# Kernel optimization log

Hardware: AMD Instinct MI355X
Metric: run time of the kernel (lower is better)

The kernel has to match this reference:

```python
import jax, jax.numpy as jnp
import numpy as np

H, DK, OUT = 8, 32, 256
SQRT_DK = float(np.sqrt(DK))


def _proj(feat, W, b):
    # (N, in) -> (N, H, DK)
    return (feat @ W + b).reshape(feat.shape[0], H, DK)


def _rel(k_src, v_src, q_dst, src, dst, att_w, msg_w, pri, n_dst):
    # HGT-style per-relation edge attention + segment softmax + aggregation.
    key = jnp.einsum('ehd,hdk->ehk', k_src[src], att_w)          # (E,H,DK)
    att = (q_dst[dst] * key).sum(-1) * pri / SQRT_DK             # (E,H)
    val = jnp.einsum('ehd,hdk->ehk', v_src[src], msg_w)          # (E,H,DK)
    m = jax.ops.segment_max(att, dst, num_segments=n_dst)
    m = jnp.where(jnp.isfinite(m), m, 0.0)
    e = jnp.exp(att - m[dst])
    s = jax.ops.segment_sum(e, dst, num_segments=n_dst)
    alpha = e / jnp.maximum(s[dst], 1e-9)
    h = jax.ops.segment_sum(alpha[..., None] * val, dst, num_segments=n_dst)
    return jax.nn.relu(h.reshape(n_dst, OUT))                    # relu per etype (reduce_func)


def _ln(x, g, b):
    mu = x.mean(-1, keepdims=True)
    var = ((x - mu) ** 2).mean(-1, keepdims=True)
    return (x - mu) / jnp.sqrt(var + 1e-5) * g + b


def _forward(feat_word, feat_topic, feat_doc, Wk, bk, Wq, bq, Wv, bv, Wa, ba,
             ln_scale, ln_bias, skip, rel_pri, rel_att, rel_msg,
             src_ww, dst_ww, src_wt, dst_wt, src_wd, dst_wd,
             src_tt, dst_tt, src_td, dst_td):
    # ntype order: word=0, topic=1, doc=2; etype order: ww=0, wt=1, wd=2, tt=3, td=4
    Nw, Nt, Nd = feat_word.shape[0], feat_topic.shape[0], feat_doc.shape[0]
    k_w, q_w, v_w = _proj(feat_word, Wk[0], bk[0]), _proj(feat_word, Wq[0], bq[0]), _proj(feat_word, Wv[0], bv[0])
    k_t, q_t, v_t = _proj(feat_topic, Wk[1], bk[1]), _proj(feat_topic, Wq[1], bq[1]), _proj(feat_topic, Wv[1], bv[1])
    q_d = _proj(feat_doc, Wq[2], bq[2])
    t_ww = _rel(k_w, v_w, q_w, src_ww, dst_ww, rel_att[0], rel_msg[0], rel_pri[0], Nw)
    t_wt = _rel(k_w, v_w, q_t, src_wt, dst_wt, rel_att[1], rel_msg[1], rel_pri[1], Nt)
    t_wd = _rel(k_w, v_w, q_d, src_wd, dst_wd, rel_att[2], rel_msg[2], rel_pri[2], Nd)
    t_tt = _rel(k_t, v_t, q_t, src_tt, dst_tt, rel_att[3], rel_msg[3], rel_pri[3], Nt)
    t_td = _rel(k_t, v_t, q_d, src_td, dst_td, rel_att[4], rel_msg[4], rel_pri[4], Nd)
    # cross_reducer='mean' across etypes targeting each ntype
    t_word, t_topic, t_doc = t_ww, (t_wt + t_tt) * 0.5, (t_wd + t_td) * 0.5
    outs = []
    for i, (t, feat) in enumerate([(t_word, feat_word), (t_topic, feat_topic), (t_doc, feat_doc)]):
        a = jax.nn.sigmoid(skip[i])
        trans = (t @ Wa[i] + ba[i]) * a + feat * (1.0 - a)
        outs.append(_ln(trans, ln_scale[i], ln_bias[i]))
    return jnp.concatenate(outs, axis=0)  # (Nw+Nt+Nd, OUT)


def setup_inputs() -> dict:
    key = jax.random.key(0)
    ks = jax.random.split(key, 32)
    Nw, Nt, Nd, D = 20000, 2000, 5000, 256
    E = {'ww': (150000, Nw, Nw), 'wt': (80000, Nw, Nt), 'wd': (80000, Nw, Nd),
         'tt': (20000, Nt, Nt), 'td': (40000, Nt, Nd)}
    inp = {
        'feat_word': jax.random.normal(ks[0], (Nw, D), jnp.float32),
        'feat_topic': jax.random.normal(ks[1], (Nt, D), jnp.float32),
        'feat_doc': jax.random.normal(ks[2], (Nd, D), jnp.float32),
        'Wk': jax.random.normal(ks[3], (3, D, D), jnp.float32) * 0.05,
        'bk': jax.random.normal(ks[4], (3, D), jnp.float32) * 0.02,
        'Wq': jax.random.normal(ks[5], (3, D, D), jnp.float32) * 0.05,
        'bq': jax.random.normal(ks[6], (3, D), jnp.float32) * 0.02,
        'Wv': jax.random.normal(ks[7], (3, D, D), jnp.float32) * 0.05,
        'bv': jax.random.normal(ks[8], (3, D), jnp.float32) * 0.02,
        'Wa': jax.random.normal(ks[9], (3, D, D), jnp.float32) * 0.05,
        'ba': jax.random.normal(ks[10], (3, D), jnp.float32) * 0.02,
        'ln_scale': jnp.ones((3, D), jnp.float32),
        'ln_bias': jnp.zeros((3, D), jnp.float32),
        'skip': jnp.ones((3,), jnp.float32),
        'rel_pri': jnp.ones((5, H), jnp.float32),
        'rel_att': jax.random.normal(ks[11], (5, H, DK, DK), jnp.float32) * 0.1,
        'rel_msg': jax.random.normal(ks[12], (5, H, DK, DK), jnp.float32) * 0.1,
    }
    for i, (et, (ne, ns, nd)) in enumerate(E.items()):
        inp['src_' + et] = jax.random.randint(ks[13 + 2 * i], (ne,), 0, ns, jnp.int32)
        inp['dst_' + et] = jax.random.randint(ks[14 + 2 * i], (ne,), 0, nd, jnp.int32)
    return inp


def reference(feat_word, feat_topic, feat_doc, Wk, bk, Wq, bq, Wv, bv, Wa, ba,
              ln_scale, ln_bias, skip, rel_pri, rel_att, rel_msg,
              src_ww, dst_ww, src_wt, dst_wt, src_wd, dst_wd,
              src_tt, dst_tt, src_td, dst_td):
    return _forward(feat_word, feat_topic, feat_doc, Wk, bk, Wq, bq, Wv, bv, Wa, ba,
                    ln_scale, ln_bias, skip, rel_pri, rel_att, rel_msg,
                    src_ww, dst_ww, src_wt, dst_wt, src_wd, dst_wd,
                    src_tt, dst_tt, src_td, dst_td)
```

## Files before the change

### kernel.cpp

```cpp
#include <hip/hip_runtime.h>

static constexpr int NW = 20000, NT = 2000, ND = 5000;
static constexpr int E_WW = 150000, E_WT = 80000, E_WD = 80000, E_TT = 20000, E_TD = 40000;

typedef short bf16x8 __attribute__((ext_vector_type(8)));
typedef float f32x4 __attribute__((ext_vector_type(4)));

__device__ __forceinline__ unsigned short f2bf(float f) {
  union { float f; unsigned int u; } c; c.f = f;
  unsigned int u = c.u;
  u += 0x7fffu + ((u >> 16) & 1u);
  return (unsigned short)(u >> 16);
}
__device__ __forceinline__ float bf2f(unsigned short h) {
  union { unsigned int u; float f; } c; c.u = ((unsigned int)h) << 16; return c.f;
}
__device__ __forceinline__ bf16x8 pack8(float4 a, float4 b) {
  bf16x8 r;
  r[0] = (short)f2bf(a.x); r[1] = (short)f2bf(a.y); r[2] = (short)f2bf(a.z); r[3] = (short)f2bf(a.w);
  r[4] = (short)f2bf(b.x); r[5] = (short)f2bf(b.y); r[6] = (short)f2bf(b.z); r[7] = (short)f2bf(b.w);
  return r;
}

struct Pack7 { const float* src[7]; unsigned short* dst[7]; };
__global__ __launch_bounds__(256) void pack_wt7(Pack7 p) {
  __shared__ float tile[32][33];
  const float* W = p.src[blockIdx.x];
  unsigned short* WT = p.dst[blockIdx.x];
  int bk = blockIdx.y * 32, bn = blockIdx.z * 32;
  int tx = threadIdx.x & 31, ty = threadIdx.x >> 5;
#pragma unroll
  for (int i = 0; i < 32; i += 8)
    tile[ty + i][tx] = W[(size_t)(bk + ty + i) * 256 + bn + tx];
  __syncthreads();
#pragma unroll
  for (int i = 0; i < 32; i += 8)
    WT[(size_t)(bn + ty + i) * 256 + bk + tx] = f2bf(tile[tx][ty + i]);
}

__global__ void pack_headw(const float* __restrict__ w, unsigned short* __restrict__ out, int nmat) {
  int t = blockIdx.x * blockDim.x + threadIdx.x;
  if (t >= nmat * 8192) return;
  int m = t >> 13, rem = t & 8191;
  int hc = rem >> 9, idx = rem & 511;
  int lane = idx >> 3, j = idx & 7;
  int h = hc >> 1, c = hc & 1;
  int k = (lane >> 4) * 8 + j, n = c * 16 + (lane & 15);
  out[t] = f2bf(w[(size_t)m * 8192 + h * 1024 + k * 32 + n]);
}

struct EffArgs {
  const float* wq[5]; const float* bq[5];
  unsigned short* dst[5];
  float* beff;
  const float* att;
};
__global__ void wq_eff_kernel(EffArgs a) {
  int t = blockIdx.x * blockDim.x + threadIdx.x;
  if (t < 5 * 65536) {
    int r = t >> 16, rem = t & 65535;
    int n = rem >> 8, kk = rem & 255;
    int h = n >> 5, j = n & 31;
    const float* wrow = a.wq[r] + kk * 256 + h * 32;
    const float* arow = a.att + r * 8192 + h * 1024 + j * 32;
    float s = 0.f;
#pragma unroll
    for (int d = 0; d < 32; d += 4) {
      float4 wv = *(const float4*)(wrow + d);
      float4 av = *(const float4*)(arow + d);
      s += wv.x * av.x + wv.y * av.y + wv.z * av.z + wv.w * av.w;
    }
    a.dst[r][n * 256 + kk] = f2bf(s);
  } else {
    int idx = t - 5 * 65536;
    if (idx < 1280) {
      int r = idx >> 8, n = idx & 255;
      int h = n >> 5, j = n & 31;
      const float* brow = a.bq[r] + h * 32;
      const float* arow = a.att + r * 8192 + h * 1024 + j * 32;
      float s = 0.f;
#pragma unroll
      for (int d = 0; d < 32; d += 4) {
        float4 bv = *(const float4*)(brow + d);
        float4 av = *(const float4*)(arow + d);
        s += bv.x * av.x + bv.y * av.y + bv.z * av.z + bv.w * av.w;
      }
      a.beff[r * 256 + n] = s;
    }
  }
}

struct ProjAll {
  const float* A[3];
  const unsigned short* WT[3];
  const float* bias[3][4];
  unsigned short* outp[3][4];
  int ostride[3][4];
  int M[3], ncolb[3], bcum[4];
};
__global__ __launch_bounds__(256) void proj_all(ProjAll pa) {
  __shared__ unsigned short As[64 * 64];
  __shared__ unsigned short Bs[64 * 64];
  int nt = 0;
  while (nt < 2 && (int)blockIdx.x >= pa.bcum[nt + 1]) nt++;
  int local = blockIdx.x - pa.bcum[nt];
  int ncolb = pa.ncolb[nt];
  int bmi = local / ncolb, bnb = local % ncolb;
  const int bm = bmi * 64, bn = bnb * 64;
  const float* A = pa.A[nt];
  const unsigned short* WT = pa.WT[nt];
  const int M = pa.M[nt];
  const int tid = threadIdx.x, wave = tid >> 6, lane = tid & 63;
  f32x4 acc[4] = {};
  const int ar = wave * 16 + (lane & 15);
  const int swz = lane & 7;
  for (int k0 = 0; k0 < 256; k0 += 64) {
#pragma unroll
    for (int i = 0; i < 2; i++) {
      int c = tid + i * 256;
      int row = c >> 3, sl = c & 7;
      int srow = bm + row;
      float4 a0 = make_float4(0.f, 0.f, 0.f, 0.f), a1 = a0;
      if (srow < M) {
        a0 = *(const float4*)(A + (size_t)srow * 256 + k0 + sl * 8);
        a1 = *(const float4*)(A + (size_t)srow * 256 + k0 + sl * 8 + 4);
      }
      *(bf16x8*)&As[row * 64 + (sl ^ (row & 7)) * 8] = pack8(a0, a1);
      bf16x8 bv = *(const bf16x8*)(WT + (size_t)(bn + row) * 256 + k0 + sl * 8);
      *(bf16x8*)&Bs[row * 64 + (sl ^ (row & 7)) * 8] = bv;
    }
    __syncthreads();
#pragma unroll
    for (int kk = 0; kk < 2; kk++) {
      int slot = kk * 4 + (lane >> 4);
      bf16x8 a = *(const bf16x8*)&As[ar * 64 + ((slot ^ swz) * 8)];
#pragma unroll
      for (int nf = 0; nf < 4; nf++) {
        int br = nf * 16 + (lane & 15);
        bf16x8 b = *(const bf16x8*)&Bs[br * 64 + ((slot ^ swz) * 8)];
        acc[nf] = __builtin_amdgcn_mfma_f32_16x16x32_bf16(a, b, acc[nf], 0, 0, 0);
      }
    }
    __syncthreads();
  }
  const int col = lane & 15;
  const int seg = bnb >> 2;
  const float* bias = pa.bias[nt][seg];
  unsigned short* outp = pa.outp[nt][seg];
  const int ostride = pa.ostride[nt][seg];
  const int cbase = (bnb & 3) * 64;
#pragma unroll
  for (int nf = 0; nf < 4; nf++) {
    float bsv = bias[cbase + nf * 16 + col];
#pragma unroll
    for (int rr = 0; rr < 4; rr++) {
      int row = bm + wave * 16 + (lane >> 4) * 4 + rr;
      if (row < M)
        outp[(size_t)row * ostride + cbase + nf * 16 + col] = f2bf(acc[nf][rr] + bsv);
    }
  }
}

struct CsrDesc {
  const int* dst[5];
  const int* src[5];
  int E[5], N[5], cbase[5];
};

__global__ void hist5(CsrDesc d, int* __restrict__ counts) {
  int t = blockIdx.x * blockDim.x + threadIdx.x;
  int r = 0, base = 0;
  while (r < 5 && t >= base + d.E[r]) { base += d.E[r]; r++; }
  if (r >= 5) return;
  int e = t - base;
  atomicAdd(counts + d.cbase[r] + d.dst[r][e], 1);
}

__global__ __launch_bounds__(1024) void scan_all(const int* __restrict__ cnt,
                                                 int* __restrict__ off, int N) {
  __shared__ int wpart[16];
  __shared__ int carry_s;
  int tid = threadIdx.x, lane = tid & 63, w = tid >> 6;
  if (tid == 0) carry_s = 0;
  __syncthreads();
  for (int base = 0; base < N; base += 4096) {
    int idx = base + tid * 4;
    int v0 = 0, v1 = 0, v2 = 0, v3 = 0;
    if (idx + 3 < N) {
      int4 t4 = *(const int4*)(cnt + idx);
      v0 = t4.x; v1 = t4.y; v2 = t4.z; v3 = t4.w;
    } else if (idx < N) {
      v0 = cnt[idx];
      if (idx + 1 < N) v1 = cnt[idx + 1];
      if (idx + 2 < N) v2 = cnt[idx + 2];
    }
    int tsum = v0 + v1 + v2 + v3;
    int x = tsum;
#pragma unroll
    for (int dlt = 1; dlt < 64; dlt <<= 1) {
      int t = __shfl_up(x, dlt, 64);
      if (lane >= dlt) x += t;
    }
    if (lane == 63) wpart[w] = x;
    __syncthreads();
    if (w == 0 && lane < 16) {
      int y = wpart[lane];
#pragma unroll
      for (int dlt = 1; dlt < 16; dlt <<= 1) {
        int t = __shfl_up(y, dlt, 64);
        if (lane >= dlt) y += t;
      }
      wpart[lane] = y;
    }
    __syncthreads();
    int excl = carry_s + ((w > 0) ? wpart[w - 1] : 0) + (x - tsum);
    if (idx < N)     off[idx]     = excl;
    if (idx + 1 < N) off[idx + 1] = excl + v0;
    if (idx + 2 < N) off[idx + 2] = excl + v0 + v1;
    if (idx + 3 < N) off[idx + 3] = excl + v0 + v1 + v2;
    __syncthreads();
    if (tid == 1023) carry_s = excl + tsum;
    __syncthreads();
  }
  if (tid == 0) off[N] = carry_s;
}

__global__ void scatter5(CsrDesc d, const int* __restrict__ offsets, int* __restrict__ cursor,
                         int* __restrict__ ssrc) {
  int t = blockIdx.x * blockDim.x + threadIdx.x;
  int r = 0, base = 0;
  while (r < 5 && t >= base + d.E[r]) { base += d.E[r]; r++; }
  if (r >= 5) return;
  int e = t - base;
  int dn = d.dst[r][e];
  int pos = offsets[d.cbase[r] + dn] + atomicAdd(cursor + d.cbase[r] + dn, 1);
  ssrc[pos] = d.src[r][e];
}

struct AttArgs {
  const unsigned short* qh[5]; const unsigned short* kv[5];
  const int* offs[5]; unsigned short* agg[5];
  const int* ssrc;
  const float* pri;
  int bcum[6]; int Ndst[5];
};
__global__ __launch_bounds__(256) void fused_att_agg(AttArgs a) {
  int r = 0;
  while (r < 4 && (int)blockIdx.x >= a.bcum[r + 1]) r++;
  int wave = threadIdx.x >> 6, lane = threadIdx.x & 63;
  int node = (blockIdx.x - a.bcum[r]) * 4 + wave;
  if (node >= a.Ndst[r]) return;
  const unsigned short* qh = a.qh[r];
  const unsigned short* kv = a.kv[r];
  const int* ssrc = a.ssrc;
  const int* offs = a.offs[r];
  int h = lane >> 3;
  float prih = a.pri[r * 8 + h] * 0.17677669529663687f;
  int r0 = offs[node], r1 = offs[node + 1];
  float4 acc = make_float4(0.f, 0.f, 0.f, 0.f);
  if (r0 < r1) {
    ushort4 qv = *(const ushort4*)(qh + (size_t)node * 256 + lane * 4);
    float q0 = bf2f(qv.x), q1 = bf2f(qv.y), q2 = bf2f(qv.z), q3 = bf2f(qv.w);
    float m = -1e30f, s = 0.f;
    for (int i = r0; i < r1; i += 2) {
      int sA = ssrc[i];
      bool two = (i + 1 < r1);
      int sB = two ? ssrc[i + 1] : sA;
      const unsigned short* pA = kv + (size_t)sA * 512 + lane * 4;
      const unsigned short* pB = kv + (size_t)sB * 512 + lane * 4;
      ushort4 kA = *(const ushort4*)pA;
      ushort4 kB = *(const ushort4*)pB;
      ushort4 vA = *(const ushort4*)(pA + 256);
      ushort4 vB = *(const ushort4*)(pB + 256);
      float dA = q0 * bf2f(kA.x) + q1 * bf2f(kA.y) + q2 * bf2f(kA.z) + q3 * bf2f(kA.w);
      float dB = q0 * bf2f(kB.x) + q1 * bf2f(kB.y) + q2 * bf2f(kB.z) + q3 * bf2f(kB.w);
      dA += __shfl_xor(dA, 1, 64); dB += __shfl_xor(dB, 1, 64);
      dA += __shfl_xor(dA, 2, 64); dB += __shfl_xor(dB, 2, 64);
      dA += __shfl_xor(dA, 4, 64); dB += __shfl_xor(dB, 4, 64);
      float lA = dA * prih;
      float lB = two ? dB * prih : -1e30f;
      float mn = fmaxf(m, fmaxf(lA, lB));
      float sc = __expf(m - mn);
      float wA = __expf(lA - mn);
      float wB = __expf(lB - mn);
      m = mn;
      s = s * sc + wA + wB;
      acc.x = acc.x * sc + wA * bf2f(vA.x) + wB * bf2f(vB.x);
      acc.y = acc.y * sc + wA * bf2f(vA.y) + wB * bf2f(vB.y);
      acc.z = acc.z * sc + wA * bf2f(vA.z) + wB * bf2f(vB.z);
      acc.w = acc.w * sc + wA * bf2f(vA.w) + wB * bf2f(vB.w);
    }
    float inv = 1.f / fmaxf(s, 1e-9f);
    acc.x *= inv; acc.y *= inv; acc.z *= inv; acc.w *= inv;
  }
  ushort4 o;
  o.x = f2bf(acc.x); o.y = f2bf(acc.y); o.z = f2bf(acc.z); o.w = f2bf(acc.w);
  *(ushort4*)(a.agg[r] + (size_t)node * 256 + lane * 4) = o;
}

struct MsgArgs {
  const unsigned short* aggA[3]; const unsigned short* aggB[3];
  const unsigned short* fA[3]; const unsigned short* fB[3];
  unsigned short* t[3];
  float scale[3];
  int N[3]; int bcum[4];
};
__global__ __launch_bounds__(256) void msg_transform_all(MsgArgs a) {
  int g = 0;
  while (g < 2 && (int)blockIdx.x >= a.bcum[g + 1]) g++;
  int local = blockIdx.x - a.bcum[g];
  const unsigned short* aggA = a.aggA[g];
  const unsigned short* aggB = a.aggB[g];
  const unsigned short* fA = a.fA[g];
  const unsigned short* fB = a.fB[g];
  unsigned short* t = a.t[g];
  float scale = a.scale[g];
  int N = a.N[g];
  int wave = threadIdx.x >> 6, lane = threadIdx.x & 63;
  int r0 = local * 64 + wave * 16;
  int arow = r0 + (lane & 15);
  bool valid = arow < N;
  int kofs = (lane >> 4) * 8;
  f32x4 z{};
#pragma unroll
  for (int h = 0; h < 8; h++) {
    bf16x8 aA{}, aB{};
    if (valid) {
      aA = *(const bf16x8*)(aggA + (size_t)arow * 256 + h * 32 + kofs);
      if (aggB) aB = *(const bf16x8*)(aggB + (size_t)arow * 256 + h * 32 + kofs);
    }
#pragma unroll
    for (int c = 0; c < 2; c++) {
      bf16x8 bA = *(const bf16x8*)(fA + ((h * 2 + c) * 64 + lane) * 8);
      f32x4 oA = __builtin_amdgcn_mfma_f32_16x16x32_bf16(aA, bA, z, 0, 0, 0);
      f32x4 oB = z;
      if (aggB) {
        bf16x8 bB = *(const bf16x8*)(fB + ((h * 2 + c) * 64 + lane) * 8);
        oB = __builtin_amdgcn_mfma_f32_16x16x32_bf16(aB, bB, z, 0, 0, 0);
      }
      int colc = h * 32 + c * 16 + (lane & 15);
#pragma unroll
      for (int rr = 0; rr < 4; rr++) {
        int row = r0 + (lane >> 4) * 4 + rr;
        if (row < N) {
          float v = fmaxf(oA[rr], 0.f) + fmaxf(oB[rr], 0.f);
          t[(size_t)row * 256 + colc] = f2bf(v * scale);
        }
      }
    }
  }
}

struct OutAll {
  const unsigned short* tA[3]; const unsigned short* WT[3];
  const float* ba[3]; const float* feat[3];
  const float* gamma[3]; const float* beta[3];
  float* op[3];
  int M[3], bcum[4];
  const float* skipv;
};
__global__ __launch_bounds__(256) void out_all_ln(OutAll oa) {
  __shared__ unsigned short As[64 * 64];
  __shared__ unsigned short Bs[256 * 64];
  int g = 0;
  while (g < 2 && (int)blockIdx.x >= oa.bcum[g + 1]) g++;
  const int bm = (blockIdx.x - oa.bcum[g]) * 64;
  const unsigned short* tA = oa.tA[g];
  const unsigned short* WT = oa.WT[g];
  const int M = oa.M[g];
  const int tid = threadIdx.x, wave = tid >> 6, lane = tid & 63;
  f32x4 acc[16] = {};
  const int ar = wave * 16 + (lane & 15);
  const int swz = lane & 7;
  for (int k0 = 0; k0 < 256; k0 += 64) {
#pragma unroll
    for (int i = 0; i < 2; i++) {
      int c = tid + i * 256;
      int row = c >> 3, sl = c & 7;
      int srow = bm + row;
      bf16x8 av{};
      if (srow < M) av = *(const bf16x8*)(tA + (size_t)srow * 256 + k0 + sl * 8);
      *(bf16x8*)&As[row * 64 + (sl ^ (row & 7)) * 8] = av;
    }
#pragma unroll
    for (int i = 0; i < 8; i++) {
      int c = tid + i * 256;
      int row = c >> 3, sl = c & 7;
      bf16x8 bv = *(const bf16x8*)(WT + (size_t)row * 256 + k0 + sl * 8);
      *(bf16x8*)&Bs[row * 64 + (sl ^ (row & 7)) * 8] = bv;
    }
    __syncthreads();
#pragma unroll
    for (int kk = 0; kk < 2; kk++) {
      int slot = kk * 4 + (lane >> 4);
      bf16x8 a = *(const bf16x8*)&As[ar * 64 + ((slot ^ swz) * 8)];
#pragma unroll
      for (int nf = 0; nf < 16; nf++) {
        int br = nf * 16 + (lane & 15);
        bf16x8 b = *(const bf16x8*)&Bs[br * 64 + ((slot ^ swz) * 8)];
        acc[nf] = __builtin_amdgcn_mfma_f32_16x16x32_bf16(a, b, acc[nf], 0, 0, 0);
      }
    }
    __syncthreads();
  }
  const int c16 = lane & 15;
  float a_skip = 1.f / (1.f + __expf(-oa.skipv[g]));
  float one_m = 1.f - a_skip;
  const float* gamma = oa.gamma[g];
  const float* beta = oa.beta[g];
  const float* ba = oa.ba[g];
  const float* feat = oa.feat[g];
  float* outp = oa.op[g];
  float gg[16], bb[16], bia[16];
#pragma unroll
  for (int nf = 0; nf < 16; nf++) {
    gg[nf] = gamma[nf * 16 + c16];
    bb[nf] = beta[nf * 16 + c16];
    bia[nf] = ba[nf * 16 + c16];
  }
#pragma unroll
  for (int rr = 0; rr < 4; rr++) {
    int row = bm + wave * 16 + (lane >> 4) * 4 + rr;
    bool valid = row < M;
#pragma unroll
    for (int nf = 0; nf < 16; nf++) {
      float fv = valid ? feat[(size_t)row * 256 + nf * 16 + c16] : 0.f;
      acc[nf][rr] = (acc[nf][rr] + bia[nf]) * a_skip + fv * one_m;
    }
    float p = 0.f;
#pragma unroll
    for (int nf = 0; nf < 16; nf++) p += acc[nf][rr];
    p += __shfl_xor(p, 1, 16); p += __shfl_xor(p, 2, 16);
    p += __shfl_xor(p, 4, 16); p += __shfl_xor(p, 8, 16);
    float mu = p * (1.f / 256.f);
    float qv = 0.f;
#pragma unroll
    for (int nf = 0; nf < 16; nf++) { float dd = acc[nf][rr] - mu; qv += dd * dd; }
    qv += __shfl_xor(qv, 1, 16); qv += __shfl_xor(qv, 2, 16);
    qv += __shfl_xor(qv, 4, 16); qv += __shfl_xor(qv, 8, 16);
    float rstd = rsqrtf(qv * (1.f / 256.f) + 1e-5f);
    if (valid) {
#pragma unroll
      for (int nf = 0; nf < 16; nf++)
        outp[(size_t)row * 256 + nf * 16 + c16] = (acc[nf][rr] - mu) * rstd * gg[nf] + bb[nf];
    }
  }
}

extern "C" void kernel_launch(void* const* d_in, const int* in_sizes, int n_in,
                              void* d_out, int out_size, void* d_ws, size_t ws_size,
                              hipStream_t stream) {
  const float* feat_w = (const float*)d_in[0];
  const float* feat_t = (const float*)d_in[1];
  const float* feat_d = (const float*)d_in[2];
  const float* Wk = (const float*)d_in[3];
  const float* bk = (const float*)d_in[4];
  const float* Wq = (const float*)d_in[5];
  const float* bq = (const float*)d_in[6];
  const float* Wv = (const float*)d_in[7];
  const float* bv = (const float*)d_in[8];
  const float* Wa = (const float*)d_in[9];
  const float* ba = (const float*)d_in[10];
  const float* ln_scale = (const float*)d_in[11];
  const float* ln_bias = (const float*)d_in[12];
  const float* skip = (const float*)d_in[13];
  const float* rel_pri = (const float*)d_in[14];
  const float* rel_att = (const float*)d_in[15];
  const float* rel_msg = (const float*)d_in[16];
  const int* src_ww = (const int*)d_in[17];
  const int* dst_ww = (const int*)d_in[18];
  const int* src_wt = (const int*)d_in[19];
  const int* dst_wt = (const int*)d_in[20];
  const int* src_wd = (const int*)d_in[21];
  const int* dst_wd = (const int*)d_in[22];
  const int* src_tt = (const int*)d_in[23];
  const int* dst_tt = (const int*)d_in[24];
  const int* src_td = (const int*)d_in[25];
  const int* dst_td = (const int*)d_in[26];
  float* out = (float*)d_out;
  float* ws = (float*)d_ws;

  size_t off = 0;
  auto allocF = [&](size_t nf) { float* p = ws + off; off += nf; return p; };
  unsigned short* kv_w = (unsigned short*)allocF(5120000);
  unsigned short* kv_t = (unsigned short*)allocF(512000);
  unsigned short* qhat0 = (unsigned short*)allocF(2560000);
  unsigned short* qhat1 = (unsigned short*)allocF(256000);
  unsigned short* qhat2 = (unsigned short*)allocF(640000);
  unsigned short* qhat3 = (unsigned short*)allocF(256000);
  unsigned short* qhat4 = (unsigned short*)allocF(640000);
  unsigned short* aggr0 = (unsigned short*)allocF(2560000);
  unsigned short* aggr1 = (unsigned short*)allocF(256000);
  unsigned short* aggr2 = (unsigned short*)allocF(640000);
  unsigned short* aggr3 = (unsigned short*)allocF(256000);
  unsigned short* aggr4 = (unsigned short*)allocF(640000);
  unsigned short* t_word  = (unsigned short*)allocF(2560000);
  unsigned short* t_topic = (unsigned short*)allocF(256000);
  unsigned short* t_doc   = (unsigned short*)allocF(640000);
  unsigned short* WTw = (unsigned short*)allocF(98304);
  unsigned short* WTt = (unsigned short*)allocF(131072);
  unsigned short* WTd = (unsigned short*)allocF(65536);
  unsigned short* WTa = (unsigned short*)allocF(98304);
  unsigned short* wvp = (unsigned short*)allocF(20480);
  float* bq_eff = allocF(1280);
  int* counts  = (int*)allocF(34000);
  int* cursor  = (int*)allocF(34000);
  int* offsets = (int*)allocF(34004);
  int* ssrc    = (int*)allocF(370000);

  dim3 b256(256);
  auto cdiv = [](int a, int b) { return (a + b - 1) / b; };

  Pack7 p7;
  p7.src[0] = Wk;           p7.dst[0] = WTw + 65536;
  p7.src[1] = Wv;           p7.dst[1] = WTw + 131072;
  p7.src[2] = Wk + 65536;   p7.dst[2] = WTt;
  p7.src[3] = Wv + 65536;   p7.dst[3] = WTt + 65536;
  p7.src[4] = Wa;           p7.dst[4] = WTa;
  p7.src[5] = Wa + 65536;   p7.dst[5] = WTa + 65536;
  p7.src[6] = Wa + 131072;  p7.dst[6] = WTa + 131072;
  pack_wt7<<<dim3(7, 8, 8), b256, 0, stream>>>(p7);
  {
    EffArgs ea;
    ea.wq[0] = Wq;           ea.bq[0] = bq;        ea.dst[0] = WTw;
    ea.wq[1] = Wq + 65536;   ea.bq[1] = bq + 256;  ea.dst[1] = WTt + 131072;
    ea.wq[2] = Wq + 131072;  ea.bq[2] = bq + 512;  ea.dst[2] = WTd;
    ea.wq[3] = Wq + 65536;   ea.bq[3] = bq + 256;  ea.dst[3] = WTt + 196608;
    ea.wq[4] = Wq + 131072;  ea.bq[4] = bq + 512;  ea.dst[4] = WTd + 65536;
    ea.beff = bq_eff;
    ea.att = rel_att;
    wq_eff_kernel<<<cdiv(5 * 65536 + 1280, 256), b256, 0, stream>>>(ea);
  }
  pack_headw<<<160, b256, 0, stream>>>(rel_msg, wvp, 5);

  CsrDesc dsc;
  dsc.dst[0] = dst_ww; dsc.dst[1] = dst_wt; dsc.dst[2] = dst_wd; dsc.dst[3] = dst_tt; dsc.dst[4] = dst_td;
  dsc.src[0] = src_ww; dsc.src[1] = src_wt; dsc.src[2] = src_wd; dsc.src[3] = src_tt; dsc.src[4] = src_td;
  int Es[5] = {E_WW, E_WT, E_WD, E_TT, E_TD};
  int Ns[5] = {NW, NT, ND, NT, ND};
  int cb = 0;
  for (int r = 0; r < 5; r++) {
    dsc.E[r] = Es[r]; dsc.N[r] = Ns[r]; dsc.cbase[r] = cb;
    cb += Ns[r];
  }
  hipMemsetAsync(counts, 0, (size_t)68000 * sizeof(int), stream);
  hist5<<<cdiv(370000, 256), b256, 0, stream>>>(dsc, counts);
  scan_all<<<1, 1024, 0, stream>>>(counts, offsets, 34000);
  scatter5<<<cdiv(370000, 256), b256, 0, stream>>>(dsc, offsets, cursor, ssrc);

  {
    ProjAll pa;
    pa.A[0] = feat_w; pa.A[1] = feat_t; pa.A[2] = feat_d;
    pa.WT[0] = WTw;   pa.WT[1] = WTt;   pa.WT[2] = WTd;
    pa.M[0] = NW; pa.M[1] = NT; pa.M[2] = ND;
    pa.bias[0][0] = bq_eff;       pa.outp[0][0] = qhat0;      pa.ostride[0][0] = 256;
    pa.bias[0][1] = bk;           pa.outp[0][1] = kv_w;       pa.ostride[0][1] = 512;
    pa.bias[0][2] = bv;           pa.outp[0][2] = kv_w + 256; pa.ostride[0][2] = 512;
    pa.bias[0][3] = bq_eff;       pa.outp[0][3] = qhat0;      pa.ostride[0][3] = 256;
    pa.bias[1][0] = bk + 256;     pa.outp[1][0] = kv_t;       pa.ostride[1][0] = 512;
    pa.bias[1][1] = bv + 256;     pa.outp[1][1] = kv_t + 256; pa.ostride[1][1] = 512;
    pa.bias[1][2] = bq_eff + 256; pa.outp[1][2] = qhat1;      pa.ostride[1][2] = 256;
    pa.bias[1][3] = bq_eff + 768; pa.outp[1][3] = qhat3;      pa.ostride[1][3] = 256;
    pa.bias[2][0] = bq_eff + 512;  pa.outp[2][0] = qhat2;     pa.ostride[2][0] = 256;
    pa.bias[2][1] = bq_eff + 1024; pa.outp[2][1] = qhat4;     pa.ostride[2][1] = 256;
    pa.bias[2][2] = bq_eff;        pa.outp[2][2] = qhat2;     pa.ostride[2][2] = 256;
    pa.bias[2][3] = bq_eff;        pa.outp[2][3] = qhat2;     pa.ostride[2][3] = 256;
    pa.ncolb[0] = 12; pa.ncolb[1] = 16; pa.ncolb[2] = 8;
    int bc = 0;
    int nb0 = cdiv(NW, 64) * 12, nb1 = cdiv(NT, 64) * 16, nb2 = cdiv(ND, 64) * 8;
    pa.bcum[0] = 0; pa.bcum[1] = nb0; pa.bcum[2] = nb0 + nb1; pa.bcum[3] = nb0 + nb1 + nb2;
    bc = pa.bcum[3];
    proj_all<<<bc, b256, 0, stream>>>(pa);
  }

  int NdstA[5] = {NW, NT, ND, NT, ND};

  {
    AttArgs aa;
    aa.qh[0] = qhat0; aa.qh[1] = qhat1; aa.qh[2] = qhat2; aa.qh[3] = qhat3; aa.qh[4] = qhat4;
    aa.kv[0] = aa.kv[1] = aa.kv[2] = kv_w; aa.kv[3] = aa.kv[4] = kv_t;
    unsigned short* aggs[5] = {aggr0, aggr1, aggr2, aggr3, aggr4};
    aa.ssrc = ssrc;
    int bc = 0;
    for (int r = 0; r < 5; r++) {
      aa.offs[r] = offsets + dsc.cbase[r];
      aa.agg[r] = aggs[r];
      aa.Ndst[r] = NdstA[r];
      aa.bcum[r] = bc; bc += cdiv(NdstA[r], 4);
    }
    aa.bcum[5] = bc;
    aa.pri = rel_pri;
    fused_att_agg<<<bc, b256, 0, stream>>>(aa);
  }

  {
    MsgArgs ma;
    ma.aggA[0] = aggr0; ma.aggB[0] = nullptr;
    ma.fA[0] = wvp;             ma.fB[0] = wvp;
    ma.t[0] = t_word;  ma.scale[0] = 1.0f;  ma.N[0] = NW;
    ma.aggA[1] = aggr1; ma.aggB[1] = aggr3;
    ma.fA[1] = wvp + 8192;      ma.fB[1] = wvp + 3 * 8192;
    ma.t[1] = t_topic; ma.scale[1] = 0.5f;  ma.N[1] = NT;
    ma.aggA[2] = aggr2; ma.aggB[2] = aggr4;
    ma.fA[2] = wvp + 2 * 8192;  ma.fB[2] = wvp + 4 * 8192;
    ma.t[2] = t_doc;   ma.scale[2] = 0.5f;  ma.N[2] = ND;
    int bc = 0;
    for (int g = 0; g < 3; g++) { ma.bcum[g] = bc; bc += cdiv(ma.N[g], 64); }
    ma.bcum[3] = bc;
    msg_transform_all<<<bc, b256, 0, stream>>>(ma);
  }

  {
    OutAll oa;
    oa.tA[0] = t_word;  oa.tA[1] = t_topic; oa.tA[2] = t_doc;
    oa.WT[0] = WTa; oa.WT[1] = WTa + 65536; oa.WT[2] = WTa + 131072;
    oa.ba[0] = ba; oa.ba[1] = ba + 256; oa.ba[2] = ba + 512;
    oa.feat[0] = feat_w; oa.feat[1] = feat_t; oa.feat[2] = feat_d;
    oa.gamma[0] = ln_scale; oa.gamma[1] = ln_scale + 256; oa.gamma[2] = ln_scale + 512;
    oa.beta[0] = ln_bias; oa.beta[1] = ln_bias + 256; oa.beta[2] = ln_bias + 512;
    oa.op[0] = out; oa.op[1] = out + (size_t)NW * 256; oa.op[2] = out + (size_t)(NW + NT) * 256;
    oa.M[0] = NW; oa.M[1] = NT; oa.M[2] = ND;
    int bc = 0;
    for (int g = 0; g < 3; g++) { oa.bcum[g] = bc; bc += cdiv(oa.M[g], 64); }
    oa.bcum[3] = bc;
    oa.skipv = skip;
    out_all_ln<<<bc, b256, 0, stream>>>(oa);
  }

  (void)in_sizes; (void)n_in; (void)out_size; (void)ws_size;
}
```

Before: 228.6 us.

## Store K/V in FP8, merge prep kernels, fold scan into projection launch

The projected key/value tensors are now stored as FP8 (e4m3 via the packed convert builtins) instead of bf16. This halves the bytes gathered per edge in the attention/aggregation kernel. The weight-packing, effective-Wq, head-weight packing and histogram kernels are merged into one prep launch, and the exclusive scan now runs as an extra block of the projection kernel, which removes several launches. FP8 storage lowers the precision of K and V and may push results past the accuracy tolerance, and the single-block 256-thread scan is serial and may stretch the projection kernel's tail.

```diff
diff --git a/kernel.cpp b/kernel.cpp
--- a/kernel.cpp
+++ b/kernel.cpp
@@ -5,6 +5,7 @@
 
 typedef short bf16x8 __attribute__((ext_vector_type(8)));
 typedef float f32x4 __attribute__((ext_vector_type(4)));
+typedef float f32x2 __attribute__((ext_vector_type(2)));
 
 __device__ __forceinline__ unsigned short f2bf(float f) {
   union { float f; unsigned int u; } c; c.f = f;
@@ -21,72 +22,94 @@
   r[4] = (short)f2bf(b.x); r[5] = (short)f2bf(b.y); r[6] = (short)f2bf(b.z); r[7] = (short)f2bf(b.w);
   return r;
 }
-
-struct Pack7 { const float* src[7]; unsigned short* dst[7]; };
-__global__ __launch_bounds__(256) void pack_wt7(Pack7 p) {
-  __shared__ float tile[32][33];
-  const float* W = p.src[blockIdx.x];
-  unsigned short* WT = p.dst[blockIdx.x];
-  int bk = blockIdx.y * 32, bn = blockIdx.z * 32;
-  int tx = threadIdx.x & 31, ty = threadIdx.x >> 5;
-#pragma unroll
-  for (int i = 0; i < 32; i += 8)
-    tile[ty + i][tx] = W[(size_t)(bk + ty + i) * 256 + bn + tx];
-  __syncthreads();
-#pragma unroll
-  for (int i = 0; i < 32; i += 8)
-    WT[(size_t)(bn + ty + i) * 256 + bk + tx] = f2bf(tile[tx][ty + i]);
-}
-
-__global__ void pack_headw(const float* __restrict__ w, unsigned short* __restrict__ out, int nmat) {
-  int t = blockIdx.x * blockDim.x + threadIdx.x;
-  if (t >= nmat * 8192) return;
-  int m = t >> 13, rem = t & 8191;
-  int hc = rem >> 9, idx = rem & 511;
-  int lane = idx >> 3, j = idx & 7;
-  int h = hc >> 1, c = hc & 1;
-  int k = (lane >> 4) * 8 + j, n = c * 16 + (lane & 15);
-  out[t] = f2bf(w[(size_t)m * 8192 + h * 1024 + k * 32 + n]);
-}
-
-struct EffArgs {
-  const float* wq[5]; const float* bq[5];
-  unsigned short* dst[5];
+__device__ __forceinline__ unsigned char f2fp8(float x) {
+  int p = __builtin_amdgcn_cvt_pk_fp8_f32(x, x, 0, false);
+  return (unsigned char)(p & 0xff);
+}
+
+struct CsrDesc {
+  const int* dst[5];
+  const int* src[5];
+  int E[5], N[5], cbase[5];
+};
+
+struct PrepArgs {
+  const float* psrc[7]; unsigned short* pdst[7];
+  const float* wq[5]; const float* bqp[5];
+  unsigned short* qdst[5];
   float* beff;
   const float* att;
+  const float* msg; unsigned short* wvp;
+  CsrDesc dsc;
+  int* counts;
+  int bEff, bHw, bHist, bTot;
 };
-__global__ void wq_eff_kernel(EffArgs a) {
-  int t = blockIdx.x * blockDim.x + threadIdx.x;
-  if (t < 5 * 65536) {
-    int r = t >> 16, rem = t & 65535;
-    int n = rem >> 8, kk = rem & 255;
-    int h = n >> 5, j = n & 31;
-    const float* wrow = a.wq[r] + kk * 256 + h * 32;
-    const float* arow = a.att + r * 8192 + h * 1024 + j * 32;
-    float s = 0.f;
-#pragma unroll
-    for (int d = 0; d < 32; d += 4) {
-      float4 wv = *(const float4*)(wrow + d);
-      float4 av = *(const float4*)(arow + d);
-      s += wv.x * av.x + wv.y * av.y + wv.z * av.z + wv.w * av.w;
-    }
-    a.dst[r][n * 256 + kk] = f2bf(s);
-  } else {
-    int idx = t - 5 * 65536;
-    if (idx < 1280) {
-      int r = idx >> 8, n = idx & 255;
+__global__ __launch_bounds__(256) void prep_kernel(PrepArgs a) {
+  __shared__ float tile[32][33];
+  int b = blockIdx.x;
+  int tid = threadIdx.x;
+  if (b < a.bEff) {
+    int m = b >> 6, bk = ((b >> 3) & 7) * 32, bn = (b & 7) * 32;
+    const float* W = a.psrc[m];
+    unsigned short* WT = a.pdst[m];
+    int tx = tid & 31, ty = tid >> 5;
+#pragma unroll
+    for (int i = 0; i < 32; i += 8)
+      tile[ty + i][tx] = W[(size_t)(bk + ty + i) * 256 + bn + tx];
+    __syncthreads();
+#pragma unroll
+    for (int i = 0; i < 32; i += 8)
+      WT[(size_t)(bn + ty + i) * 256 + bk + tx] = f2bf(tile[tx][ty + i]);
+  } else if (b < a.bHw) {
+    int t = (b - a.bEff) * 256 + tid;
+    if (t < 5 * 65536) {
+      int r = t >> 16, rem = t & 65535;
+      int n = rem >> 8, kk = rem & 255;
       int h = n >> 5, j = n & 31;
-      const float* brow = a.bq[r] + h * 32;
+      const float* wrow = a.wq[r] + kk * 256 + h * 32;
       const float* arow = a.att + r * 8192 + h * 1024 + j * 32;
       float s = 0.f;
 #pragma unroll
       for (int d = 0; d < 32; d += 4) {
-        float4 bv = *(const float4*)(brow + d);
+        float4 wv = *(const float4*)(wrow + d);
         float4 av = *(const float4*)(arow + d);
-        s += bv.x * av.x + bv.y * av.y + bv.z * av.z + bv.w * av.w;
-      }
-      a.beff[r * 256 + n] = s;
-    }
+        s += wv.x * av.x + wv.y * av.y + wv.z * av.z + wv.w * av.w;
+      }
+      a.qdst[r][n * 256 + kk] = f2bf(s);
+    } else {
+      int idx = t - 5 * 65536;
+      if (idx < 1280) {
+        int r = idx >> 8, n = idx & 255;
+        int h = n >> 5, j = n & 31;
+        const float* brow = a.bqp[r] + h * 32;
+        const float* arow = a.att + r * 8192 + h * 1024 + j * 32;
+        float s = 0.f;
+#pragma unroll
+        for (int d = 0; d < 32; d += 4) {
+          float4 bv = *(const float4*)(brow + d);
+          float4 av = *(const float4*)(arow + d);
+          s += bv.x * av.x + bv.y * av.y + bv.z * av.z + bv.w * av.w;
+        }
+        a.beff[r * 256 + n] = s;
+      }
+    }
+  } else if (b < a.bHist) {
+    int t = (b - a.bHw) * 256 + tid;
+    if (t < 5 * 8192) {
+      int m = t >> 13, rem = t & 8191;
+      int hc = rem >> 9, idx = rem & 511;
+      int lane = idx >> 3, j = idx & 7;
+      int h = hc >> 1, c = hc & 1;
+      int k = (lane >> 4) * 8 + j, n = c * 16 + (lane & 15);
+      a.wvp[t] = f2bf(a.msg[(size_t)m * 8192 + h * 1024 + k * 32 + n]);
+    }
+  } else {
+    int t = (b - a.bHist) * 256 + tid;
+    int r = 0, base = 0;
+    while (r < 5 && t >= base + a.dsc.E[r]) { base += a.dsc.E[r]; r++; }
+    if (r >= 5) return;
+    int e = t - base;
+    atomicAdd(a.counts + a.dsc.cbase[r] + a.dsc.dst[r][e], 1);
   }
 }
 
@@ -94,13 +117,60 @@
   const float* A[3];
   const unsigned short* WT[3];
   const float* bias[3][4];
-  unsigned short* outp[3][4];
-  int ostride[3][4];
+  unsigned char* outB[3][4];
+  int esz[3][4];
   int M[3], ncolb[3], bcum[4];
+  const int* counts; int* offsets; int scanN;
 };
 __global__ __launch_bounds__(256) void proj_all(ProjAll pa) {
   __shared__ unsigned short As[64 * 64];
   __shared__ unsigned short Bs[64 * 64];
+  __shared__ int wpart2[4];
+  __shared__ int carry2;
+  const int tid = threadIdx.x;
+  if ((int)blockIdx.x >= pa.bcum[3]) {
+    int lane = tid & 63, w = tid >> 6;
+    if (tid == 0) carry2 = 0;
+    __syncthreads();
+    const int N = pa.scanN;
+    for (int base = 0; base < N; base += 1024) {
+      int idx = base + tid * 4;
+      int v0 = 0, v1 = 0, v2 = 0, v3 = 0;
+      if (idx + 3 < N) {
+        int4 t4 = *(const int4*)(pa.counts + idx);
+        v0 = t4.x; v1 = t4.y; v2 = t4.z; v3 = t4.w;
+      } else if (idx < N) {
+        v0 = pa.counts[idx];
+        if (idx + 1 < N) v1 = pa.counts[idx + 1];
+        if (idx + 2 < N) v2 = pa.counts[idx + 2];
+      }
+      int ts = v0 + v1 + v2 + v3;
+      int x = ts;
+#pragma unroll
+      for (int d = 1; d < 64; d <<= 1) {
+        int t = __shfl_up(x, d, 64);
+        if (lane >= d) x += t;
+      }
+      if (lane == 63) wpart2[w] = x;
+      __syncthreads();
+      if (tid == 0) {
+        int s = 0;
+#pragma unroll
+        for (int j = 0; j < 4; j++) { int t = wpart2[j]; wpart2[j] = s; s += t; }
+      }
+      __syncthreads();
+      int excl = carry2 + wpart2[w] + (x - ts);
+      if (idx < N)     pa.offsets[idx]     = excl;
+      if (idx + 1 < N) pa.offsets[idx + 1] = excl + v0;
+      if (idx + 2 < N) pa.offsets[idx + 2] = excl + v0 + v1;
+      if (idx + 3 < N) pa.offsets[idx + 3] = excl + v0 + v1 + v2;
+      __syncthreads();
+      if (tid == 255) carry2 = excl + ts;
+      __syncthreads();
+    }
+    if (tid == 0) pa.offsets[N] = carry2;
+    return;
+  }
   int nt = 0;
   while (nt < 2 && (int)blockIdx.x >= pa.bcum[nt + 1]) nt++;
   int local = blockIdx.x - pa.bcum[nt];
@@ -110,7 +180,7 @@
   const float* A = pa.A[nt];
   const unsigned short* WT = pa.WT[nt];
   const int M = pa.M[nt];
-  const int tid = threadIdx.x, wave = tid >> 6, lane = tid & 63;
+  const int wave = tid >> 6, lane = tid & 63;
   f32x4 acc[4] = {};
   const int ar = wave * 16 + (lane & 15);
   const int swz = lane & 7;
@@ -133,12 +203,12 @@
 #pragma unroll
     for (int kk = 0; kk < 2; kk++) {
       int slot = kk * 4 + (lane >> 4);
-      bf16x8 a = *(const bf16x8*)&As[ar * 64 + ((slot ^ swz) * 8)];
+      bf16x8 av = *(const bf16x8*)&As[ar * 64 + ((slot ^ swz) * 8)];
 #pragma unroll
       for (int nf = 0; nf < 4; nf++) {
         int br = nf * 16 + (lane & 15);
-        bf16x8 b = *(const bf16x8*)&Bs[br * 64 + ((slot ^ swz) * 8)];
-        acc[nf] = __builtin_amdgcn_mfma_f32_16x16x32_bf16(a, b, acc[nf], 0, 0, 0);
+        bf16x8 bv = *(const bf16x8*)&Bs[br * 64 + ((slot ^ swz) * 8)];
+        acc[nf] = __builtin_amdgcn_mfma_f32_16x16x32_bf16(av, bv, acc[nf], 0, 0, 0);
       }
     }
     __syncthreads();
@@ -146,83 +216,23 @@
   const int col = lane & 15;
   const int seg = bnb >> 2;
   const float* bias = pa.bias[nt][seg];
-  unsigned short* outp = pa.outp[nt][seg];
-  const int ostride = pa.ostride[nt][seg];
+  unsigned char* outB = pa.outB[nt][seg];
+  const int esz = pa.esz[nt][seg];
   const int cbase = (bnb & 3) * 64;
 #pragma unroll
   for (int nf = 0; nf < 4; nf++) {
     float bsv = bias[cbase + nf * 16 + col];
+    int idx = cbase + nf * 16 + col;
 #pragma unroll
     for (int rr = 0; rr < 4; rr++) {
       int row = bm + wave * 16 + (lane >> 4) * 4 + rr;
-      if (row < M)
-        outp[(size_t)row * ostride + cbase + nf * 16 + col] = f2bf(acc[nf][rr] + bsv);
-    }
-  }
-}
-
-struct CsrDesc {
-  const int* dst[5];
-  const int* src[5];
-  int E[5], N[5], cbase[5];
-};
-
-__global__ void hist5(CsrDesc d, int* __restrict__ counts) {
-  int t = blockIdx.x * blockDim.x + threadIdx.x;
-  int r = 0, base = 0;
-  while (r < 5 && t >= base + d.E[r]) { base += d.E[r]; r++; }
-  if (r >= 5) return;
-  int e = t - base;
-  atomicAdd(counts + d.cbase[r] + d.dst[r][e], 1);
-}
-
-__global__ __launch_bounds__(1024) void scan_all(const int* __restrict__ cnt,
-                                                 int* __restrict__ off, int N) {
-  __shared__ int wpart[16];
-  __shared__ int carry_s;
-  int tid = threadIdx.x, lane = tid & 63, w = tid >> 6;
-  if (tid == 0) carry_s = 0;
-  __syncthreads();
-  for (int base = 0; base < N; base += 4096) {
-    int idx = base + tid * 4;
-    int v0 = 0, v1 = 0, v2 = 0, v3 = 0;
-    if (idx + 3 < N) {
-      int4 t4 = *(const int4*)(cnt + idx);
-      v0 = t4.x; v1 = t4.y; v2 = t4.z; v3 = t4.w;
-    } else if (idx < N) {
-      v0 = cnt[idx];
-      if (idx + 1 < N) v1 = cnt[idx + 1];
-      if (idx + 2 < N) v2 = cnt[idx + 2];
-    }
-    int tsum = v0 + v1 + v2 + v3;
-    int x = tsum;
-#pragma unroll
-    for (int dlt = 1; dlt < 64; dlt <<= 1) {
-      int t = __shfl_up(x, dlt, 64);
-      if (lane >= dlt) x += t;
-    }
-    if (lane == 63) wpart[w] = x;
-    __syncthreads();
-    if (w == 0 && lane < 16) {
-      int y = wpart[lane];
-#pragma unroll
-      for (int dlt = 1; dlt < 16; dlt <<= 1) {
-        int t = __shfl_up(y, dlt, 64);
-        if (lane >= dlt) y += t;
-      }
-      wpart[lane] = y;
-    }
-    __syncthreads();
-    int excl = carry_s + ((w > 0) ? wpart[w - 1] : 0) + (x - tsum);
-    if (idx < N)     off[idx]     = excl;
-    if (idx + 1 < N) off[idx + 1] = excl + v0;
-    if (idx + 2 < N) off[idx + 2] = excl + v0 + v1;
-    if (idx + 3 < N) off[idx + 3] = excl + v0 + v1 + v2;
-    __syncthreads();
-    if (tid == 1023) carry_s = excl + tsum;
-    __syncthreads();
-  }
-  if (tid == 0) off[N] = carry_s;
+      if (row < M) {
+        float v = acc[nf][rr] + bsv;
+        if (esz == 2) *(unsigned short*)(outB + (size_t)row * 512 + idx * 2) = f2bf(v);
+        else          outB[(size_t)row * 512 + idx] = f2fp8(v);
+      }
+    }
+  }
 }
 
 __global__ void scatter5(CsrDesc d, const int* __restrict__ offsets, int* __restrict__ cursor,
@@ -238,7 +248,7 @@
 }
 
 struct AttArgs {
-  const unsigned short* qh[5]; const unsigned short* kv[5];
+  const unsigned short* qh[5]; const unsigned char* kv8[5];
   const int* offs[5]; unsigned short* agg[5];
   const int* ssrc;
   const float* pri;
@@ -251,7 +261,7 @@
   int node = (blockIdx.x - a.bcum[r]) * 4 + wave;
   if (node >= a.Ndst[r]) return;
   const unsigned short* qh = a.qh[r];
-  const unsigned short* kv = a.kv[r];
+  const unsigned char* kvb = a.kv8[r];
   const int* ssrc = a.ssrc;
   const int* offs = a.offs[r];
   int h = lane >> 3;
@@ -266,14 +276,18 @@
       int sA = ssrc[i];
       bool two = (i + 1 < r1);
       int sB = two ? ssrc[i + 1] : sA;
-      const unsigned short* pA = kv + (size_t)sA * 512 + lane * 4;
-      const unsigned short* pB = kv + (size_t)sB * 512 + lane * 4;
-      ushort4 kA = *(const ushort4*)pA;
-      ushort4 kB = *(const ushort4*)pB;
-      ushort4 vA = *(const ushort4*)(pA + 256);
-      ushort4 vB = *(const ushort4*)(pB + 256);
-      float dA = q0 * bf2f(kA.x) + q1 * bf2f(kA.y) + q2 * bf2f(kA.z) + q3 * bf2f(kA.w);
-      float dB = q0 * bf2f(kB.x) + q1 * bf2f(kB.y) + q2 * bf2f(kB.z) + q3 * bf2f(kB.w);
+      const unsigned char* pA = kvb + (size_t)sA * 512 + lane * 4;
+      const unsigned char* pB = kvb + (size_t)sB * 512 + lane * 4;
+      unsigned int kuA = *(const unsigned int*)pA;
+      unsigned int kuB = *(const unsigned int*)pB;
+      unsigned int vuA = *(const unsigned int*)(pA + 256);
+      unsigned int vuB = *(const unsigned int*)(pB + 256);
+      f32x2 ka01 = __builtin_amdgcn_cvt_pk_f32_fp8((int)kuA, false);
+      f32x2 ka23 = __builtin_amdgcn_cvt_pk_f32_fp8((int)kuA, true);
+      f32x2 kb01 = __builtin_amdgcn_cvt_pk_f32_fp8((int)kuB, false);
+      f32x2 kb23 = __builtin_amdgcn_cvt_pk_f32_fp8((int)kuB, true);
+      float dA = q0 * ka01[0] + q1 * ka01[1] + q2 * ka23[0] + q3 * ka23[1];
+      float dB = q0 * kb01[0] + q1 * kb01[1] + q2 * kb23[0] + q3 * kb23[1];
       dA += __shfl_xor(dA, 1, 64); dB += __shfl_xor(dB, 1, 64);
       dA += __shfl_xor(dA, 2, 64); dB += __shfl_xor(dB, 2, 64);
       dA += __shfl_xor(dA, 4, 64); dB += __shfl_xor(dB, 4, 64);
@@ -285,10 +299,14 @@
       float wB = __expf(lB - mn);
       m = mn;
       s = s * sc + wA + wB;
-      acc.x = acc.x * sc + wA * bf2f(vA.x) + wB * bf2f(vB.x);
-      acc.y = acc.y * sc + wA * bf2f(vA.y) + wB * bf2f(vB.y);
-      acc.z = acc.z * sc + wA * bf2f(vA.z) + wB * bf2f(vB.z);
-      acc.w = acc.w * sc + wA * bf2f(vA.w) + wB * bf2f(vB.w);
+      f32x2 va01 = __builtin_amdgcn_cvt_pk_f32_fp8((int)vuA, false);
+      f32x2 va23 = __builtin_amdgcn_cvt_pk_f32_fp8((int)vuA, true);
+      f32x2 vb01 = __builtin_amdgcn_cvt_pk_f32_fp8((int)vuB, false);
+      f32x2 vb23 = __builtin_amdgcn_cvt_pk_f32_fp8((int)vuB, true);
+      acc.x = acc.x * sc + wA * va01[0] + wB * vb01[0];
+      acc.y = acc.y * sc + wA * va01[1] + wB * vb01[1];
+      acc.z = acc.z * sc + wA * va23[0] + wB * vb23[0];
+      acc.w = acc.w * sc + wA * va23[1] + wB * vb23[1];
     }
     float inv = 1.f / fmaxf(s, 1e-9f);
     acc.x *= inv; acc.y *= inv; acc.z *= inv; acc.w *= inv;
@@ -393,12 +411,12 @@
 #pragma unroll
     for (int kk = 0; kk < 2; kk++) {
       int slot = kk * 4 + (lane >> 4);
-      bf16x8 a = *(const bf16x8*)&As[ar * 64 + ((slot ^ swz) * 8)];
+      bf16x8 av = *(const bf16x8*)&As[ar * 64 + ((slot ^ swz) * 8)];
 #pragma unroll
       for (int nf = 0; nf < 16; nf++) {
         int br = nf * 16 + (lane & 15);
-        bf16x8 b = *(const bf16x8*)&Bs[br * 64 + ((slot ^ swz) * 8)];
-        acc[nf] = __builtin_amdgcn_mfma_f32_16x16x32_bf16(a, b, acc[nf], 0, 0, 0);
+        bf16x8 bv = *(const bf16x8*)&Bs[br * 64 + ((slot ^ swz) * 8)];
+        acc[nf] = __builtin_amdgcn_mfma_f32_16x16x32_bf16(av, bv, acc[nf], 0, 0, 0);
       }
     }
     __syncthreads();
@@ -482,8 +500,8 @@
 
   size_t off = 0;
   auto allocF = [&](size_t nf) { float* p = ws + off; off += nf; return p; };
-  unsigned short* kv_w = (unsigned short*)allocF(5120000);
-  unsigned short* kv_t = (unsigned short*)allocF(512000);
+  unsigned char* kv_w = (unsigned char*)allocF(2560000);
+  unsigned char* kv_t = (unsigned char*)allocF(256000);
   unsigned short* qhat0 = (unsigned short*)allocF(2560000);
   unsigned short* qhat1 = (unsigned short*)allocF(256000);
   unsigned short* qhat2 = (unsigned short*)allocF(640000);
@@ -511,28 +529,6 @@
   dim3 b256(256);
   auto cdiv = [](int a, int b) { return (a + b - 1) / b; };
 
-  Pack7 p7;
-  p7.src[0] = Wk;           p7.dst[0] = WTw + 65536;
-  p7.src[1] = Wv;           p7.dst[1] = WTw + 131072;
-  p7.src[2] = Wk + 65536;   p7.dst[2] = WTt;
-  p7.src[3] = Wv + 65536;   p7.dst[3] = WTt + 65536;
-  p7.src[4] = Wa;           p7.dst[4] = WTa;
-  p7.src[5] = Wa + 65536;   p7.dst[5] = WTa + 65536;
-  p7.src[6] = Wa + 131072;  p7.dst[6] = WTa + 131072;
-  pack_wt7<<<dim3(7, 8, 8), b256, 0, stream>>>(p7);
-  {
-    EffArgs ea;
-    ea.wq[0] = Wq;           ea.bq[0] = bq;        ea.dst[0] = WTw;
-    ea.wq[1] = Wq + 65536;   ea.bq[1] = bq + 256;  ea.dst[1] = WTt + 131072;
-    ea.wq[2] = Wq + 131072;  ea.bq[2] = bq + 512;  ea.dst[2] = WTd;
-    ea.wq[3] = Wq + 65536;   ea.bq[3] = bq + 256;  ea.dst[3] = WTt + 196608;
-    ea.wq[4] = Wq + 131072;  ea.bq[4] = bq + 512;  ea.dst[4] = WTd + 65536;
-    ea.beff = bq_eff;
-    ea.att = rel_att;
-    wq_eff_kernel<<<cdiv(5 * 65536 + 1280, 256), b256, 0, stream>>>(ea);
-  }
-  pack_headw<<<160, b256, 0, stream>>>(rel_msg, wvp, 5);
-
   CsrDesc dsc;
   dsc.dst[0] = dst_ww; dsc.dst[1] = dst_wt; dsc.dst[2] = dst_wd; dsc.dst[3] = dst_tt; dsc.dst[4] = dst_td;
   dsc.src[0] = src_ww; dsc.src[1] = src_wt; dsc.src[2] = src_wd; dsc.src[3] = src_tt; dsc.src[4] = src_td;
@@ -543,42 +539,70 @@
     dsc.E[r] = Es[r]; dsc.N[r] = Ns[r]; dsc.cbase[r] = cb;
     cb += Ns[r];
   }
+
   hipMemsetAsync(counts, 0, (size_t)68000 * sizeof(int), stream);
-  hist5<<<cdiv(370000, 256), b256, 0, stream>>>(dsc, counts);
-  scan_all<<<1, 1024, 0, stream>>>(counts, offsets, 34000);
-  scatter5<<<cdiv(370000, 256), b256, 0, stream>>>(dsc, offsets, cursor, ssrc);
+
+  {
+    PrepArgs pr;
+    pr.psrc[0] = Wk;           pr.pdst[0] = WTw + 65536;
+    pr.psrc[1] = Wv;           pr.pdst[1] = WTw + 131072;
+    pr.psrc[2] = Wk + 65536;   pr.pdst[2] = WTt;
+    pr.psrc[3] = Wv + 65536;   pr.pdst[3] = WTt + 65536;
+    pr.psrc[4] = Wa;           pr.pdst[4] = WTa;
+    pr.psrc[5] = Wa + 65536;   pr.pdst[5] = WTa + 65536;
+    pr.psrc[6] = Wa + 131072;  pr.pdst[6] = WTa + 131072;
+    pr.wq[0] = Wq;           pr.bqp[0] = bq;        pr.qdst[0] = WTw;
+    pr.wq[1] = Wq + 65536;   pr.bqp[1] = bq + 256;  pr.qdst[1] = WTt + 131072;
+    pr.wq[2] = Wq + 131072;  pr.bqp[2] = bq + 512;  pr.qdst[2] = WTd;
+    pr.wq[3] = Wq + 65536;   pr.bqp[3] = bq + 256;  pr.qdst[3] = WTt + 196608;
+    pr.wq[4] = Wq + 131072;  pr.bqp[4] = bq + 512;  pr.qdst[4] = WTd + 65536;
+    pr.beff = bq_eff;
+    pr.att = rel_att;
+    pr.msg = rel_msg; pr.wvp = wvp;
+    pr.dsc = dsc; pr.counts = counts;
+    int nPack = 7 * 64;
+    int nEff  = cdiv(5 * 65536 + 1280, 256);
+    int nHw   = cdiv(5 * 8192, 256);
+    int nHist = cdiv(370000, 256);
+    pr.bEff  = nPack;
+    pr.bHw   = nPack + nEff;
+    pr.bHist = nPack + nEff + nHw;
+    pr.bTot  = nPack + nEff + nHw + nHist;
+    prep_kernel<<<pr.bTot, b256, 0, stream>>>(pr);
+  }
 
   {
     ProjAll pa;
     pa.A[0] = feat_w; pa.A[1] = feat_t; pa.A[2] = feat_d;
     pa.WT[0] = WTw;   pa.WT[1] = WTt;   pa.WT[2] = WTd;
     pa.M[0] = NW; pa.M[1] = NT; pa.M[2] = ND;
-    pa.bias[0][0] = bq_eff;       pa.outp[0][0] = qhat0;      pa.ostride[0][0] = 256;
-    pa.bias[0][1] = bk;           pa.outp[0][1] = kv_w;       pa.ostride[0][1] = 512;
-    pa.bias[0][2] = bv;           pa.outp[0][2] = kv_w + 256; pa.ostride[0][2] = 512;
-    pa.bias[0][3] = bq_eff;       pa.outp[0][3] = qhat0;      pa.ostride[0][3] = 256;
-    pa.bias[1][0] = bk + 256;     pa.outp[1][0] = kv_t;       pa.ostride[1][0] = 512;
-    pa.bias[1][1] = bv + 256;     pa.outp[1][1] = kv_t + 256; pa.ostride[1][1] = 512;
-    pa.bias[1][2] = bq_eff + 256; pa.outp[1][2] = qhat1;      pa.ostride[1][2] = 256;
-    pa.bias[1][3] = bq_eff + 768; pa.outp[1][3] = qhat3;      pa.ostride[1][3] = 256;
-    pa.bias[2][0] = bq_eff + 512;  pa.outp[2][0] = qhat2;     pa.ostride[2][0] = 256;
-    pa.bias[2][1] = bq_eff + 1024; pa.outp[2][1] = qhat4;     pa.ostride[2][1] = 256;
-    pa.bias[2][2] = bq_eff;        pa.outp[2][2] = qhat2;     pa.ostride[2][2] = 256;
-    pa.bias[2][3] = bq_eff;        pa.outp[2][3] = qhat2;     pa.ostride[2][3] = 256;
+    pa.bias[0][0] = bq_eff;       pa.outB[0][0] = (unsigned char*)qhat0; pa.esz[0][0] = 2;
+    pa.bias[0][1] = bk;           pa.outB[0][1] = kv_w;                  pa.esz[0][1] = 1;
+    pa.bias[0][2] = bv;           pa.outB[0][2] = kv_w + 256;            pa.esz[0][2] = 1;
+    pa.bias[0][3] = bq_eff;       pa.outB[0][3] = (unsigned char*)qhat0; pa.esz[0][3] = 2;
+    pa.bias[1][0] = bk + 256;     pa.outB[1][0] = kv_t;                  pa.esz[1][0] = 1;
+    pa.bias[1][1] = bv + 256;     pa.outB[1][1] = kv_t + 256;            pa.esz[1][1] = 1;
+    pa.bias[1][2] = bq_eff + 256; pa.outB[1][2] = (unsigned char*)qhat1; pa.esz[1][2] = 2;
+    pa.bias[1][3] = bq_eff + 768; pa.outB[1][3] = (unsigned char*)qhat3; pa.esz[1][3] = 2;
+    pa.bias[2][0] = bq_eff + 512;  pa.outB[2][0] = (unsigned char*)qhat2; pa.esz[2][0] = 2;
+    pa.bias[2][1] = bq_eff + 1024; pa.outB[2][1] = (unsigned char*)qhat4; pa.esz[2][1] = 2;
+    pa.bias[2][2] = bq_eff;        pa.outB[2][2] = (unsigned char*)qhat2; pa.esz[2][2] = 2;
+    pa.bias[2][3] = bq_eff;        pa.outB[2][3] = (unsigned char*)qhat2; pa.esz[2][3] = 2;
     pa.ncolb[0] = 12; pa.ncolb[1] = 16; pa.ncolb[2] = 8;
-    int bc = 0;
     int nb0 = cdiv(NW, 64) * 12, nb1 = cdiv(NT, 64) * 16, nb2 = cdiv(ND, 64) * 8;
     pa.bcum[0] = 0; pa.bcum[1] = nb0; pa.bcum[2] = nb0 + nb1; pa.bcum[3] = nb0 + nb1 + nb2;
-    bc = pa.bcum[3];
-    proj_all<<<bc, b256, 0, stream>>>(pa);
-  }
+    pa.counts = counts; pa.offsets = offsets; pa.scanN = 34000;
+    proj_all<<<pa.bcum[3] + 1, b256, 0, stream>>>(pa);
+  }
+
+  scatter5<<<cdiv(370000, 256), b256, 0, stream>>>(dsc, offsets, cursor, ssrc);
 
   int NdstA[5] = {NW, NT, ND, NT, ND};
 
   {
     AttArgs aa;
     aa.qh[0] = qhat0; aa.qh[1] = qhat1; aa.qh[2] = qhat2; aa.qh[3] = qhat3; aa.qh[4] = qhat4;
-    aa.kv[0] = aa.kv[1] = aa.kv[2] = kv_w; aa.kv[3] = aa.kv[4] = kv_t;
+    aa.kv8[0] = aa.kv8[1] = aa.kv8[2] = kv_w; aa.kv8[3] = aa.kv8[4] = kv_t;
     unsigned short* aggs[5] = {aggr0, aggr1, aggr2, aggr3, aggr4};
     aa.ssrc = ssrc;
     int bc = 0;
```

After: 209.0 us. 1.09x faster.
